# Optimization experiments

Measured on AMD Instinct MI355X. Metric: run time of the kernel, lower is better.

## Reference

```python
import jax, jax.numpy as jnp
import numpy as np

N_EMB = 1024
HEAD_SIZE = 128

def setup_inputs() -> dict:
    key = jax.random.key(0)
    kx, kq, kk, kv = jax.random.split(key, 4)
    s = 1.0 / np.sqrt(N_EMB)
    return {
        "x": jax.random.normal(kx, (4, 4096, N_EMB), dtype=jnp.float32),
        "Wq": jax.random.normal(kq, (N_EMB, HEAD_SIZE), dtype=jnp.float32) * s,
        "Wk": jax.random.normal(kk, (N_EMB, HEAD_SIZE), dtype=jnp.float32) * s,
        "Wv": jax.random.normal(kv, (N_EMB, HEAD_SIZE), dtype=jnp.float32) * s,
    }

def reference(x, Wq, Wk, Wv) -> jnp.ndarray:
    B, T, C = x.shape
    q = jnp.einsum('btc,cd->btd', x, Wq)  # [B,T,H]
    k = jnp.einsum('btc,cd->btd', x, Wk)
    v = jnp.einsum('btc,cd->btd', x, Wv)
    # NOTE: original scales by sqrt(n_emb), not sqrt(head_size)
    wei = jnp.einsum('btd,bsd->bts', q, k) / jnp.sqrt(jnp.asarray(C, x.dtype))
    causal = jnp.tril(jnp.ones((T, T), dtype=bool))
    wei = jnp.where(causal, wei, -jnp.inf)
    wei = jax.nn.softmax(wei, axis=-1)
    return jnp.einsum('bts,bsd->btd', wei, v)
```

## Files before the change

kernel.cpp:

```cpp
#include <hip/hip_runtime.h>
#include <hip/hip_bf16.h>


#define TSEQ 4096
#define NBATCH 4
#define CEMB 1024
#define HS 128
#define NWORK 272

typedef float  f32x4  __attribute__((ext_vector_type(4)));
typedef float  f32x16 __attribute__((ext_vector_type(16)));
typedef __bf16 bf16x4 __attribute__((ext_vector_type(4)));
typedef __bf16 bf16x8 __attribute__((ext_vector_type(8)));
typedef int    i32x2  __attribute__((ext_vector_type(2)));
typedef int    i32x4  __attribute__((ext_vector_type(4)));

__device__ __forceinline__ __bf16 f2b(float f) { return (__bf16)f; }
__device__ __forceinline__ float fexp2(float f) { return __builtin_amdgcn_exp2f(f); }

__global__ void wtrans_kernel(const float* __restrict__ Wq,
                              const float* __restrict__ Wk,
                              const float* __restrict__ Wv,
                              __bf16* __restrict__ Wt) {
  const float* W = (blockIdx.y == 0) ? Wq : (blockIdx.y == 1) ? Wk : Wv;
  int g  = blockIdx.x * 256 + threadIdx.x;
  int n  = g & 127;
  int k0 = (g >> 7) * 8;
  bf16x8 v;
#pragma unroll
  for (int i = 0; i < 8; ++i) v[i] = f2b(W[(size_t)(k0 + i) * HS + n]);
  *(bf16x8*)(Wt + (size_t)blockIdx.y * HS * CEMB + (size_t)n * CEMB + k0) = v;
}

__global__ __launch_bounds__(256)
void proj_kernel(const float* __restrict__ x, const __bf16* __restrict__ Wt,
                 __bf16* __restrict__ qb, __bf16* __restrict__ kb,
                 __bf16* __restrict__ vt) {
  __shared__ __align__(16) __bf16 As[64 * 72];
  __shared__ __align__(16) __bf16 Bs[64 * 72];

  const int tid  = threadIdx.x;
  const int lane = tid & 63;
  const int w    = tid >> 6;
  const int l31  = lane & 31;
  const int half = lane >> 5;

  const int bid   = blockIdx.x;
  const int xcd   = bid & 7;
  const int rest  = bid >> 3;
  const int sub   = rest % 6;
  const int mat   = sub >> 1;
  const int nh    = sub & 1;
  const int mslab = rest / 6;
  const int m0    = (xcd + 8 * mslab) * 64;
  const int n0    = nh * 64;
  const __bf16* Wm = Wt + (size_t)mat * HS * CEMB + (size_t)n0 * CEMB;

  const int wm0 = 32 * (w & 1);
  const int wn0 = 32 * (w >> 1);

  f32x16 acc;
#pragma unroll
  for (int r = 0; r < 16; ++r) acc[r] = 0.f;

  const int srow = tid >> 3;
  const int soff = tid & 7;

  for (int ks = 0; ks < CEMB; ks += 64) {
    __syncthreads();
#pragma unroll
    for (int i = 0; i < 2; ++i) {
      int r = srow + 32 * i;
      const float* p = x + (size_t)(m0 + r) * CEMB + ks + soff * 8;
      f32x4 a = *(const f32x4*)p;
      f32x4 b = *(const f32x4*)(p + 4);
      bf16x8 h;
#pragma unroll
      for (int j = 0; j < 4; ++j) { h[j] = f2b(a[j]); h[4 + j] = f2b(b[j]); }
      *(bf16x8*)(As + r * 72 + soff * 8) = h;
    }
#pragma unroll
    for (int i = 0; i < 2; ++i) {
      int r = srow + 32 * i;
      bf16x8 v = *(const bf16x8*)(Wm + (size_t)r * CEMB + ks + soff * 8);
      *(bf16x8*)(Bs + r * 72 + soff * 8) = v;
    }
    __syncthreads();
#pragma unroll
    for (int kc = 0; kc < 4; ++kc) {
      bf16x8 af = *(const bf16x8*)(As + (wm0 + l31) * 72 + kc * 16 + half * 8);
      bf16x8 bf = *(const bf16x8*)(Bs + (wn0 + l31) * 72 + kc * 16 + half * 8);
      acc = __builtin_amdgcn_mfma_f32_32x32x16_bf16(af, bf, acc, 0, 0, 0);
    }
  }

  const int n = n0 + wn0 + l31;
  const float qscale = 1.4426950408889634f / 32.0f;
  if (mat == 0) {
#pragma unroll
    for (int r = 0; r < 16; ++r) {
      int m = m0 + wm0 + (r & 3) + 8 * (r >> 2) + 4 * half;
      qb[(size_t)m * HS + n] = f2b(acc[r] * qscale);
    }
  } else if (mat == 1) {
#pragma unroll
    for (int r = 0; r < 16; ++r) {
      int m = m0 + wm0 + (r & 3) + 8 * (r >> 2) + 4 * half;
      kb[(size_t)m * HS + n] = f2b(acc[r]);
    }
  } else {
    const int bt = m0 >> 12;
#pragma unroll
    for (int g = 0; g < 4; ++g) {
      bf16x4 pk;
#pragma unroll
      for (int d = 0; d < 4; ++d) pk[d] = f2b(acc[4 * g + d]);
      int tl = ((m0 + wm0) & 4095) + 8 * g + 4 * half;
      *(bf16x4*)(vt + ((size_t)bt * HS + n) * TSEQ + tl) = pk;
    }
  }
}

__global__ __launch_bounds__(256)
void attn_kernel(const __bf16* __restrict__ qb, const __bf16* __restrict__ kb,
                 const __bf16* __restrict__ vt,
                 __bf16* __restrict__ Opart, float* __restrict__ Lpart) {
  __shared__ __align__(16) __bf16 Kt[64 * 136];
  __shared__ __align__(16) __bf16 Vtl[128 * 72];

  const int tid   = threadIdx.x;
  const int lane  = tid & 63;
  const int w     = tid >> 6;
  const int l31   = lane & 31;
  const int half  = lane >> 5;
  const int batch = blockIdx.y;
  const int xw    = blockIdx.x;

  int q = 0;
  while (q < 31 && xw >= (((q + 2) * (q + 2)) >> 2)) ++q;
  const int split = xw - (((q + 1) * (q + 1)) >> 2);
  const int ntile = 2 * (q + 1);
  const int nsp   = (q + 2) >> 1;
  const int tps   = (ntile + nsp - 1) / nsp;
  const int it0   = split * tps;
  const int it1   = min(it0 + tps, ntile);

  const int strip0 = q * 128 + w * 32;
  const size_t bbase = (size_t)batch * TSEQ;

  bf16x8 qf[8];
  {
    const __bf16* qr = qb + (bbase + strip0 + l31) * HS + half * 8;
#pragma unroll
    for (int kc = 0; kc < 8; ++kc) qf[kc] = *(const bf16x8*)(qr + kc * 16);
  }

  f32x16 o[4];
#pragma unroll
  for (int nt = 0; nt < 4; ++nt)
#pragma unroll
    for (int r = 0; r < 16; ++r) o[nt][r] = 0.f;
  float lsum = 0.f;

  for (int it = it0; it < it1; ++it) {
    const int c0 = it * 64;
    __syncthreads();
    {
      const __bf16* src = kb + (bbase + c0) * HS;
#pragma unroll
      for (int i = 0; i < 4; ++i) {
        int c = tid + i * 256;
        int row = c >> 4, off = c & 15;
        *(bf16x8*)(&Kt[row * 136 + off * 8]) =
            *(const bf16x8*)(src + row * HS + off * 8);
      }
      const __bf16* vsrc = vt + (size_t)batch * HS * TSEQ + c0;
#pragma unroll
      for (int i = 0; i < 4; ++i) {
        int c = tid + i * 256;
        int n = c >> 3, off = c & 7;
        *(bf16x8*)(&Vtl[n * 72 + off * 8]) =
            *(const bf16x8*)(vsrc + (size_t)n * TSEQ + off * 8);
      }
    }
    __syncthreads();

    if (c0 <= strip0 + 31) {
      i32x2 pkt[2][4];
#pragma unroll
      for (int t = 0; t < 2; ++t)
#pragma unroll
        for (int j = 0; j < 4; ++j) pkt[t][j] = (i32x2){0, 0};

#pragma unroll
      for (int t = 0; t < 2; ++t) {
        if (c0 + t * 32 <= strip0 + 31) {
          f32x16 s;
#pragma unroll
          for (int r = 0; r < 16; ++r) s[r] = 0.f;
#pragma unroll
          for (int kc = 0; kc < 8; ++kc) {
            bf16x8 kf = *(const bf16x8*)(&Kt[(t * 32 + l31) * 136 + kc * 16 + half * 8]);
            s = __builtin_amdgcn_mfma_f32_32x32x16_bf16(kf, qf[kc], s, 0, 0, 0);
          }
          if (c0 + t * 32 + 31 > strip0) {
#pragma unroll
            for (int r = 0; r < 16; ++r) {
              int key = c0 + t * 32 + (r & 3) + 8 * (r >> 2) + 4 * half;
              if (key > strip0 + l31) s[r] = -INFINITY;
            }
          }
          float p[16], ps = 0.f;
#pragma unroll
          for (int r = 0; r < 16; ++r) { p[r] = fexp2(s[r]); ps += p[r]; }
          lsum += ps;
#pragma unroll
          for (int j = 0; j < 4; ++j) {
            bf16x4 t4;
#pragma unroll
            for (int d = 0; d < 4; ++d) t4[d] = f2b(p[4 * j + d]);
            pkt[t][j] = __builtin_bit_cast(i32x2, t4);
          }
        }
      }
#pragma unroll
      for (int kk = 0; kk < 4; ++kk) {
        int t = kk >> 1, lo = (kk & 1) * 2;
        i32x2 a = pkt[t][lo], b = pkt[t][lo + 1];
        i32x2 ra, rb;
        ra.x = __shfl_xor(a.x, 32); ra.y = __shfl_xor(a.y, 32);
        rb.x = __shfl_xor(b.x, 32); rb.y = __shfl_xor(b.y, 32);
        i32x4 af4;
        af4.x = half ? rb.x : a.x;
        af4.y = half ? rb.y : a.y;
        af4.z = half ? b.x  : ra.x;
        af4.w = half ? b.y  : ra.y;
        bf16x8 af = __builtin_bit_cast(bf16x8, af4);
#pragma unroll
        for (int nt = 0; nt < 4; ++nt) {
          bf16x8 vf = *(const bf16x8*)(&Vtl[(nt * 32 + l31) * 72 + kk * 16 + half * 8]);
          o[nt] = __builtin_amdgcn_mfma_f32_32x32x16_bf16(af, vf, o[nt], 0, 0, 0);
        }
      }
    }
  }

  const size_t widx = (size_t)batch * NWORK + xw;
  __bf16* Op = Opart + widx * (128 * 128);
#pragma unroll
  for (int r = 0; r < 16; ++r) {
    int rloc = w * 32 + 4 * half + (r & 3) + 8 * (r >> 2);
#pragma unroll
    for (int nt = 0; nt < 4; ++nt)
      Op[rloc * 128 + nt * 32 + l31] = f2b(o[nt][r]);
  }
  lsum += __shfl_xor(lsum, 32);
  if (half == 0) Lpart[widx * 128 + w * 32 + l31] = lsum;
}

__global__ __launch_bounds__(256)
void reduce_kernel(const __bf16* __restrict__ Opart, const float* __restrict__ Lpart,
                   float* __restrict__ out) {
  const int batch = blockIdx.y;
  const int rowg  = blockIdx.x * 8 + (threadIdx.x >> 5);
  const int q = rowg >> 7;
  const int nsp = (q + 2) >> 1;
  const int off = ((q + 1) * (q + 1)) >> 2;
  const size_t wbase = (size_t)batch * NWORK + off;
  const int row128 = rowg & 127;
  const int c0 = (threadIdx.x & 31) * 4;

  float l = 0.f;
  for (int s = 0; s < nsp; ++s) l += Lpart[(wbase + s) * 128 + row128];
  const float inv = 1.0f / l;

  const __bf16* op = Opart + wbase * (128 * 128) + row128 * 128 + c0;
  f32x4 a = {0.f, 0.f, 0.f, 0.f};
  for (int s = 0; s < nsp; ++s) {
    bf16x4 v = *(const bf16x4*)(op + (size_t)s * 128 * 128);
#pragma unroll
    for (int j = 0; j < 4; ++j) a[j] += (float)v[j];
  }
  a *= inv;
  *(f32x4*)(out + ((size_t)batch * TSEQ + rowg) * HS + c0) = a;
}

extern "C" void kernel_launch(void* const* d_in, const int* in_sizes, int n_in,
                              void* d_out, int out_size, void* d_ws, size_t ws_size,
                              hipStream_t stream) {
  const float* x  = (const float*)d_in[0];
  const float* Wq = (const float*)d_in[1];
  const float* Wk = (const float*)d_in[2];
  const float* Wv = (const float*)d_in[3];
  float* out = (float*)d_out;

  char* ws = (char*)d_ws;
  __bf16* Wt = (__bf16*)ws;
  __bf16* qb = (__bf16*)(ws + 786432);
  __bf16* kb = (__bf16*)(ws + 786432 + 4194304);
  __bf16* vt = (__bf16*)(ws + 786432 + 2 * 4194304);
  __bf16* Opart = (__bf16*)(ws + 786432 + 3 * 4194304);
  float*  Lpart = (float*)(ws + 786432 + 3 * 4194304 +
                           (size_t)NBATCH * NWORK * 128 * 128 * 2);

  wtrans_kernel<<<dim3(64, 3), 256, 0, stream>>>(Wq, Wk, Wv, Wt);
  proj_kernel<<<dim3(1536), 256, 0, stream>>>(x, Wt, qb, kb, vt);
  attn_kernel<<<dim3(NWORK, NBATCH), 256, 0, stream>>>(qb, kb, vt, Opart, Lpart);
  reduce_kernel<<<dim3(512, NBATCH), 256, 0, stream>>>(Opart, Lpart, out);
}
```

Before: 176.9 us.

## Widen projection tiles to full head width and prefetch next K-slab into registers

The projection kernel now computes a 64x128 output tile per block with 2 waves, each wave holding a 2x2 grid of 32x32 MFMA accumulators. This halves the grid and removes the duplicate x loads and fp32-to-bf16 conversions that came from splitting N into two halves. It also adds register prefetch of the next K-slab of x and W, overlapping global loads with MFMA work. In exchange it uses more registers per thread and fewer waves per block, which may lower occupancy and latency hiding.

```diff
diff --git a/kernel.cpp b/kernel.cpp
--- a/kernel.cpp
+++ b/kernel.cpp
@@ -32,12 +32,12 @@
   *(bf16x8*)(Wt + (size_t)blockIdx.y * HS * CEMB + (size_t)n * CEMB + k0) = v;
 }
 
-__global__ __launch_bounds__(256)
+__global__ __launch_bounds__(128)
 void proj_kernel(const float* __restrict__ x, const __bf16* __restrict__ Wt,
                  __bf16* __restrict__ qb, __bf16* __restrict__ kb,
                  __bf16* __restrict__ vt) {
   __shared__ __align__(16) __bf16 As[64 * 72];
-  __shared__ __align__(16) __bf16 Bs[64 * 72];
+  __shared__ __align__(16) __bf16 Bs[128 * 72];
 
   const int tid  = threadIdx.x;
   const int lane = tid & 63;
@@ -48,76 +48,120 @@
   const int bid   = blockIdx.x;
   const int xcd   = bid & 7;
   const int rest  = bid >> 3;
-  const int sub   = rest % 6;
-  const int mat   = sub >> 1;
-  const int nh    = sub & 1;
-  const int mslab = rest / 6;
+  const int mat   = rest % 3;
+  const int mslab = rest / 3;
   const int m0    = (xcd + 8 * mslab) * 64;
-  const int n0    = nh * 64;
-  const __bf16* Wm = Wt + (size_t)mat * HS * CEMB + (size_t)n0 * CEMB;
-
-  const int wm0 = 32 * (w & 1);
-  const int wn0 = 32 * (w >> 1);
-
-  f32x16 acc;
-#pragma unroll
-  for (int r = 0; r < 16; ++r) acc[r] = 0.f;
+  const __bf16* Wm = Wt + (size_t)mat * HS * CEMB;
+
+  f32x16 acc[2][2];
+#pragma unroll
+  for (int a = 0; a < 2; ++a)
+#pragma unroll
+    for (int b = 0; b < 2; ++b)
+#pragma unroll
+      for (int r = 0; r < 16; ++r) acc[a][b][r] = 0.f;
 
   const int srow = tid >> 3;
   const int soff = tid & 7;
 
+  f32x4  pa[4][2];
+  bf16x8 pb[8];
+#pragma unroll
+  for (int i = 0; i < 4; ++i) {
+    const float* p = x + (size_t)(m0 + srow + 16 * i) * CEMB + soff * 8;
+    pa[i][0] = *(const f32x4*)p;
+    pa[i][1] = *(const f32x4*)(p + 4);
+  }
+#pragma unroll
+  for (int i = 0; i < 8; ++i)
+    pb[i] = *(const bf16x8*)(Wm + (size_t)(srow + 16 * i) * CEMB + soff * 8);
+
   for (int ks = 0; ks < CEMB; ks += 64) {
     __syncthreads();
 #pragma unroll
-    for (int i = 0; i < 2; ++i) {
-      int r = srow + 32 * i;
-      const float* p = x + (size_t)(m0 + r) * CEMB + ks + soff * 8;
-      f32x4 a = *(const f32x4*)p;
-      f32x4 b = *(const f32x4*)(p + 4);
+    for (int i = 0; i < 4; ++i) {
       bf16x8 h;
 #pragma unroll
-      for (int j = 0; j < 4; ++j) { h[j] = f2b(a[j]); h[4 + j] = f2b(b[j]); }
-      *(bf16x8*)(As + r * 72 + soff * 8) = h;
-    }
-#pragma unroll
-    for (int i = 0; i < 2; ++i) {
-      int r = srow + 32 * i;
-      bf16x8 v = *(const bf16x8*)(Wm + (size_t)r * CEMB + ks + soff * 8);
-      *(bf16x8*)(Bs + r * 72 + soff * 8) = v;
-    }
+      for (int j = 0; j < 4; ++j) {
+        h[j]     = f2b(pa[i][0][j]);
+        h[4 + j] = f2b(pa[i][1][j]);
+      }
+      *(bf16x8*)(As + (srow + 16 * i) * 72 + soff * 8) = h;
+    }
+#pragma unroll
+    for (int i = 0; i < 8; ++i)
+      *(bf16x8*)(Bs + (srow + 16 * i) * 72 + soff * 8) = pb[i];
     __syncthreads();
+    if (ks + 64 < CEMB) {
+#pragma unroll
+      for (int i = 0; i < 4; ++i) {
+        const float* p = x + (size_t)(m0 + srow + 16 * i) * CEMB + ks + 64 + soff * 8;
+        pa[i][0] = *(const f32x4*)p;
+        pa[i][1] = *(const f32x4*)(p + 4);
+      }
+#pragma unroll
+      for (int i = 0; i < 8; ++i)
+        pb[i] = *(const bf16x8*)(Wm + (size_t)(srow + 16 * i) * CEMB + ks + 64 + soff * 8);
+    }
 #pragma unroll
     for (int kc = 0; kc < 4; ++kc) {
-      bf16x8 af = *(const bf16x8*)(As + (wm0 + l31) * 72 + kc * 16 + half * 8);
-      bf16x8 bf = *(const bf16x8*)(Bs + (wn0 + l31) * 72 + kc * 16 + half * 8);
-      acc = __builtin_amdgcn_mfma_f32_32x32x16_bf16(af, bf, acc, 0, 0, 0);
-    }
-  }
-
-  const int n = n0 + wn0 + l31;
+      bf16x8 af[2], bf[2];
+#pragma unroll
+      for (int mi = 0; mi < 2; ++mi)
+        af[mi] = *(const bf16x8*)(As + (mi * 32 + l31) * 72 + kc * 16 + half * 8);
+#pragma unroll
+      for (int ni = 0; ni < 2; ++ni)
+        bf[ni] = *(const bf16x8*)(Bs + (64 * w + ni * 32 + l31) * 72 + kc * 16 + half * 8);
+#pragma unroll
+      for (int mi = 0; mi < 2; ++mi)
+#pragma unroll
+        for (int ni = 0; ni < 2; ++ni)
+          acc[mi][ni] = __builtin_amdgcn_mfma_f32_32x32x16_bf16(
+              af[mi], bf[ni], acc[mi][ni], 0, 0, 0);
+    }
+  }
+
   const float qscale = 1.4426950408889634f / 32.0f;
   if (mat == 0) {
 #pragma unroll
-    for (int r = 0; r < 16; ++r) {
-      int m = m0 + wm0 + (r & 3) + 8 * (r >> 2) + 4 * half;
-      qb[(size_t)m * HS + n] = f2b(acc[r] * qscale);
-    }
+    for (int mi = 0; mi < 2; ++mi)
+#pragma unroll
+      for (int ni = 0; ni < 2; ++ni) {
+        int n = 64 * w + ni * 32 + l31;
+#pragma unroll
+        for (int r = 0; r < 16; ++r) {
+          int m = m0 + mi * 32 + (r & 3) + 8 * (r >> 2) + 4 * half;
+          qb[(size_t)m * HS + n] = f2b(acc[mi][ni][r] * qscale);
+        }
+      }
   } else if (mat == 1) {
 #pragma unroll
-    for (int r = 0; r < 16; ++r) {
-      int m = m0 + wm0 + (r & 3) + 8 * (r >> 2) + 4 * half;
-      kb[(size_t)m * HS + n] = f2b(acc[r]);
-    }
+    for (int mi = 0; mi < 2; ++mi)
+#pragma unroll
+      for (int ni = 0; ni < 2; ++ni) {
+        int n = 64 * w + ni * 32 + l31;
+#pragma unroll
+        for (int r = 0; r < 16; ++r) {
+          int m = m0 + mi * 32 + (r & 3) + 8 * (r >> 2) + 4 * half;
+          kb[(size_t)m * HS + n] = f2b(acc[mi][ni][r]);
+        }
+      }
   } else {
     const int bt = m0 >> 12;
 #pragma unroll
-    for (int g = 0; g < 4; ++g) {
-      bf16x4 pk;
-#pragma unroll
-      for (int d = 0; d < 4; ++d) pk[d] = f2b(acc[4 * g + d]);
-      int tl = ((m0 + wm0) & 4095) + 8 * g + 4 * half;
-      *(bf16x4*)(vt + ((size_t)bt * HS + n) * TSEQ + tl) = pk;
-    }
+    for (int mi = 0; mi < 2; ++mi)
+#pragma unroll
+      for (int ni = 0; ni < 2; ++ni) {
+        int n = 64 * w + ni * 32 + l31;
+#pragma unroll
+        for (int g = 0; g < 4; ++g) {
+          bf16x4 pk;
+#pragma unroll
+          for (int d = 0; d < 4; ++d) pk[d] = f2b(acc[mi][ni][4 * g + d]);
+          int tl = ((m0 + mi * 32) & 4095) + 8 * g + 4 * half;
+          *(bf16x4*)(vt + ((size_t)bt * HS + n) * TSEQ + tl) = pk;
+        }
+      }
   }
 }
 
@@ -304,7 +348,7 @@
                            (size_t)NBATCH * NWORK * 128 * 128 * 2);
 
   wtrans_kernel<<<dim3(64, 3), 256, 0, stream>>>(Wq, Wk, Wv, Wt);
-  proj_kernel<<<dim3(1536), 256, 0, stream>>>(x, Wt, qb, kb, vt);
+  proj_kernel<<<dim3(768), 128, 0, stream>>>(x, Wt, qb, kb, vt);
   attn_kernel<<<dim3(NWORK, NBATCH), 256, 0, stream>>>(qb, kb, vt, Opart, Lpart);
   reduce_kernel<<<dim3(512, NBATCH), 256, 0, stream>>>(Opart, Lpart, out);
 }
```

Result: faster. 167.5 us (-5.3%).
